# Kernel tuning notes

Hardware: AMD Instinct MI355X
Metric: run time of the kernel (lower is better)

Reference implementation:

```python
import jax, jax.numpy as jnp
import numpy as np

# Module hyperparameters (init_kwargs)
FS = 30.0          # sampling rate (Hz)
HIGH_PASS = 40.0   # bpm
LOW_PASS = 250.0   # bpm
DELTA_T = 300      # crop length (samples)
K = 64             # crops per (batch, channel)
B, C, T = 256, 16, 9000

NBINS = DELTA_T // 2 + 1  # rfft bins
# freqs = linspace(0, Fs/2, NBINS); band mask is static given shapes
_freqs = np.linspace(0.0, FS / 2.0, NBINS)
MASK_IDX = np.where((_freqs >= HIGH_PASS / 60.0) & (_freqs <= LOW_PASS / 60.0))[0]


def setup_inputs() -> dict:
    key = jax.random.key(0)
    k1, k2 = jax.random.split(key)
    inp = jax.random.normal(k1, (B, C, T), dtype=jnp.float32)
    # random temporal offsets, one per (b, c, k) crop
    offsets = jax.random.randint(k2, (B, C, K), 0, T - DELTA_T + 1, dtype=jnp.int32)
    return {"input": inp, "offsets": offsets}


def reference(input, offsets):
    # Batched gather of all random crops: [B, C, K, DELTA_T]
    t_idx = offsets[..., None] + jnp.arange(DELTA_T, dtype=jnp.int32)  # [B,C,K,dt]
    crops = jnp.take_along_axis(input[:, :, None, :], t_idx, axis=-1)
    # Remove per-crop mean
    crops = crops - jnp.mean(crops, axis=-1, keepdims=True)
    # rFFT with 'forward' norm (divide by n), power spectrum
    spec = jnp.fft.rfft(crops, axis=-1, norm='forward')   # [B,C,K,NBINS] complex
    power = spec.real ** 2 + spec.imag ** 2               # [B,C,K,NBINS]
    # Keep only the heart-rate band (static index set), normalize to unit sum
    power = power[..., MASK_IDX]                          # [B,C,K,F_band]
    power = power / jnp.sum(power, axis=-1, keepdims=True)
    return power
```

## Files before the change

### kernel.cpp

```cpp
#include <hip/hip_runtime.h>
#include <math.h>

#define TT 9000
#define DT 300
#define KK 64
#define NB 35
#define KMIN 7
#define NCH 4096
#define NPAIR (KK * NB)


typedef __bf16 bf16;
typedef __attribute__((ext_vector_type(8))) __bf16 bf16x8;
typedef __attribute__((ext_vector_type(4))) __bf16 bf16x4;
typedef __attribute__((ext_vector_type(4))) float f32x4;

#define NFRAG_ELEMS (10 * 6 * 64 * 8)

__global__ void build_w(bf16* __restrict__ tab) {
    int i = blockIdx.x * blockDim.x + threadIdx.x;
    if (i >= NFRAG_ELEMS) return;
    int j    = i & 7;
    int l    = (i >> 3) & 63;
    int f    = i >> 9;
    int nt   = f % 6;
    int ks   = f / 6;
    int quad = l >> 4;
    int c    = l & 15;
    int k    = ks * 32 + quad * 8 + j;
    int jf   = (nt % 3) * 16 + c;
    float v = 0.0f;
    if (jf <= NB - 1 && k < DT) {
        int bin = jf + KMIN;
        int ph  = (bin * k) % DT;
        float ang = 0.02094395102393195f * (float)ph;
        v = (nt >= 3) ? sinf(ang) : cosf(ang);
    }
    tab[i] = (bf16)v;
}

#define SPAD 9024

__global__ __launch_bounds__(256, 8) void st_mfma(
        const float* __restrict__ input,
        const int*   __restrict__ offsets,
        const bf16*  __restrict__ tab,
        float*       __restrict__ out) {
    __shared__ __align__(16) bf16 sig[SPAD];
    __shared__ int offs[KK];

    const int bc  = blockIdx.x;
    const int tid = threadIdx.x;

    const float4* src = (const float4*)(input + (size_t)bc * TT);
#pragma unroll
    for (int i = 0; i < 9; ++i) {
        int idx = tid + i * 256;
        if (idx < TT / 4) {
            float4 v = src[idx];
            bf16x4 b;
            b[0] = (bf16)v.x; b[1] = (bf16)v.y; b[2] = (bf16)v.z; b[3] = (bf16)v.w;
            *(bf16x4*)(sig + idx * 4) = b;
        }
    }
    if (tid < SPAD - TT) sig[TT + tid] = (bf16)0.0f;
    if (tid < KK) offs[tid] = offsets[bc * KK + tid];
    __syncthreads();

    const int w    = tid >> 6;
    const int lane = tid & 63;
    const int quad = lane >> 4;
    const int c    = lane & 15;

    const int off = offs[w * 16 + c];
    const int d0  = (off + quad * 8) >> 1;
    const unsigned sh = (unsigned)((off & 1) << 4);
    const int* ip = (const int*)sig;

    const bf16x8* wt = (const bf16x8*)tab;

    f32x4 acc[6];
#pragma unroll
    for (int nt = 0; nt < 6; ++nt) acc[nt] = (f32x4){0.f, 0.f, 0.f, 0.f};

#pragma unroll
    for (int ks = 0; ks < 10; ++ks) {
        const int db = d0 + ks * 16;
        int dw0 = ip[db + 0], dw1 = ip[db + 1], dw2 = ip[db + 2],
            dw3 = ip[db + 3], dw4 = ip[db + 4];
        union { unsigned u[4]; bf16x8 v; } a;
        a.u[0] = __builtin_amdgcn_alignbit((unsigned)dw1, (unsigned)dw0, sh);
        a.u[1] = __builtin_amdgcn_alignbit((unsigned)dw2, (unsigned)dw1, sh);
        a.u[2] = __builtin_amdgcn_alignbit((unsigned)dw3, (unsigned)dw2, sh);
        a.u[3] = __builtin_amdgcn_alignbit((unsigned)dw4, (unsigned)dw3, sh);

#pragma unroll
        for (int nt = 0; nt < 6; ++nt)
            acc[nt] = __builtin_amdgcn_mfma_f32_16x16x32_bf16(
                a.v, wt[(ks * 6 + nt) * 64 + lane], acc[nt], 0, 0, 0);
    }

    float* o = out + (size_t)bc * NPAIR;
#pragma unroll
    for (int r = 0; r < 4; ++r) {
        float p0 = acc[0][r] * acc[0][r] + acc[3][r] * acc[3][r];
        float p1 = acc[1][r] * acc[1][r] + acc[4][r] * acc[4][r];
        float p2 = acc[2][r] * acc[2][r] + acc[5][r] * acc[5][r];
        float s = p0 + p1 + ((c <= 2) ? p2 : 0.0f);
#pragma unroll
        for (int d = 1; d < 16; d <<= 1) s += __shfl_xor(s, d, 64);
        float rinv = 1.0f / s;
        int crop = w * 16 + quad * 4 + r;
        float* oc = o + crop * NB;
        oc[c] = p0 * rinv;
        oc[16 + c] = p1 * rinv;
        if (c <= 2) oc[32 + c] = p2 * rinv;
    }
}

extern "C" void kernel_launch(void* const* d_in, const int* in_sizes, int n_in,
                              void* d_out, int out_size, void* d_ws, size_t ws_size,
                              hipStream_t stream) {
    const float* input   = (const float*)d_in[0];
    const int*   offsets = (const int*)d_in[1];
    float*       out     = (float*)d_out;
    bf16*        tab     = (bf16*)d_ws;

    build_w<<<(NFRAG_ELEMS + 255) / 256, 256, 0, stream>>>(tab);
    st_mfma<<<NCH, 256, 0, stream>>>(input, offsets, tab, out);
}
```

Measured before the change: 251.2 us.

## Split frequency tiles across 12 waves and stage DFT weights in LDS

Each block grows from 4 to 12 waves. Each wave now handles one crop group and one of three frequency groups, computing only a cos/sin MFMA pair per k-step instead of six MFMAs. The bf16 DFT weight table is copied into shared memory with global_load_lds, so each wave no longer reads fragments from global memory. Per-crop normalization sums are combined across waves through a small shared array and a second barrier, and the reciprocal uses rcpf. In exchange, each block now loads about 60 KB of weights and uses far more LDS, which caps how many blocks fit on a CU, and the extra barrier adds a sync point.

```diff
diff --git a/kernel.cpp b/kernel.cpp
--- a/kernel.cpp
+++ b/kernel.cpp
@@ -16,6 +16,7 @@
 typedef __attribute__((ext_vector_type(4))) float f32x4;
 
 #define NFRAG_ELEMS (10 * 6 * 64 * 8)
+#define WBYTES 61440
 
 __global__ void build_w(bf16* __restrict__ tab) {
     int i = blockIdx.x * blockDim.x + threadIdx.x;
@@ -41,21 +42,34 @@
 
 #define SPAD 9024
 
-__global__ __launch_bounds__(256, 8) void st_mfma(
+__global__ __launch_bounds__(768, 6) void st_mfma(
         const float* __restrict__ input,
         const int*   __restrict__ offsets,
         const bf16*  __restrict__ tab,
         float*       __restrict__ out) {
     __shared__ __align__(16) bf16 sig[SPAD];
+    __shared__ __align__(16) unsigned char wlds[WBYTES];
+    __shared__ __align__(16) float part[KK][3];
     __shared__ int offs[KK];
 
-    const int bc  = blockIdx.x;
-    const int tid = threadIdx.x;
+    const int bc   = blockIdx.x;
+    const int tid  = threadIdx.x;
+    const int wid  = tid >> 6;
+    const int lane = tid & 63;
+
+#pragma unroll
+    for (int i = 0; i < 5; ++i) {
+        int chunk = wid * 5 + i;
+        __builtin_amdgcn_global_load_lds(
+            (const __attribute__((address_space(1))) void*)((const unsigned char*)tab + chunk * 1024 + lane * 16),
+            (__attribute__((address_space(3))) void*)(wlds + chunk * 1024),
+            16, 0, 0);
+    }
 
     const float4* src = (const float4*)(input + (size_t)bc * TT);
 #pragma unroll
-    for (int i = 0; i < 9; ++i) {
-        int idx = tid + i * 256;
+    for (int i = 0; i < 3; ++i) {
+        int idx = tid + i * 768;
         if (idx < TT / 4) {
             float4 v = src[idx];
             bf16x4 b;
@@ -67,21 +81,19 @@
     if (tid < KK) offs[tid] = offsets[bc * KK + tid];
     __syncthreads();
 
-    const int w    = tid >> 6;
-    const int lane = tid & 63;
+    const int m    = wid & 3;
+    const int pg   = wid >> 2;
     const int quad = lane >> 4;
     const int c    = lane & 15;
 
-    const int off = offs[w * 16 + c];
+    const int off = offs[m * 16 + c];
     const int d0  = (off + quad * 8) >> 1;
     const unsigned sh = (unsigned)((off & 1) << 4);
     const int* ip = (const int*)sig;
 
-    const bf16x8* wt = (const bf16x8*)tab;
+    const unsigned char* wp = wlds + (size_t)(pg * 64 + lane) * 16;
 
-    f32x4 acc[6];
-#pragma unroll
-    for (int nt = 0; nt < 6; ++nt) acc[nt] = (f32x4){0.f, 0.f, 0.f, 0.f};
+    f32x4 acc_c = {0.f,0.f,0.f,0.f}, acc_s = {0.f,0.f,0.f,0.f};
 
 #pragma unroll
     for (int ks = 0; ks < 10; ++ks) {
@@ -94,27 +106,32 @@
         a.u[2] = __builtin_amdgcn_alignbit((unsigned)dw3, (unsigned)dw2, sh);
         a.u[3] = __builtin_amdgcn_alignbit((unsigned)dw4, (unsigned)dw3, sh);
 
-#pragma unroll
-        for (int nt = 0; nt < 6; ++nt)
-            acc[nt] = __builtin_amdgcn_mfma_f32_16x16x32_bf16(
-                a.v, wt[(ks * 6 + nt) * 64 + lane], acc[nt], 0, 0, 0);
+        bf16x8 wc = *(const bf16x8*)(wp + (ks * 6    ) * 1024);
+        bf16x8 wn = *(const bf16x8*)(wp + (ks * 6 + 3) * 1024);
+        acc_c = __builtin_amdgcn_mfma_f32_16x16x32_bf16(a.v, wc, acc_c, 0, 0, 0);
+        acc_s = __builtin_amdgcn_mfma_f32_16x16x32_bf16(a.v, wn, acc_s, 0, 0, 0);
     }
 
-    float* o = out + (size_t)bc * NPAIR;
+    float pv[4];
 #pragma unroll
     for (int r = 0; r < 4; ++r) {
-        float p0 = acc[0][r] * acc[0][r] + acc[3][r] * acc[3][r];
-        float p1 = acc[1][r] * acc[1][r] + acc[4][r] * acc[4][r];
-        float p2 = acc[2][r] * acc[2][r] + acc[5][r] * acc[5][r];
-        float s = p0 + p1 + ((c <= 2) ? p2 : 0.0f);
+        float p = acc_c[r] * acc_c[r] + acc_s[r] * acc_s[r];
+        pv[r] = p;
+        float s = p;
 #pragma unroll
         for (int d = 1; d < 16; d <<= 1) s += __shfl_xor(s, d, 64);
-        float rinv = 1.0f / s;
-        int crop = w * 16 + quad * 4 + r;
-        float* oc = o + crop * NB;
-        oc[c] = p0 * rinv;
-        oc[16 + c] = p1 * rinv;
-        if (c <= 2) oc[32 + c] = p2 * rinv;
+        if (c == 0) part[m * 16 + quad * 4 + r][pg] = s;
+    }
+    __syncthreads();
+
+    float* ob = out + (size_t)bc * NPAIR;
+#pragma unroll
+    for (int r = 0; r < 4; ++r) {
+        int crop = m * 16 + quad * 4 + r;
+        float s = part[crop][0] + part[crop][1] + part[crop][2];
+        float rinv = __builtin_amdgcn_rcpf(s);
+        if (pg < 2 || c < 3)
+            ob[crop * NB + pg * 16 + c] = pv[r] * rinv;
     }
 }
 
@@ -127,5 +144,5 @@
     bf16*        tab     = (bf16*)d_ws;
 
     build_w<<<(NFRAG_ELEMS + 255) / 256, 256, 0, stream>>>(tab);
-    st_mfma<<<NCH, 256, 0, stream>>>(input, offsets, tab, out);
+    st_mfma<<<NCH, 768, 0, stream>>>(input, offsets, tab, out);
 }
```

New measurement: 233.2 us. -7.2%, faster.

## Stage DFT weight table in LDS and process eight channels per block

Applied to the files above, without the earlier changes.

Each block now copies the full bf16 DFT fragment table into shared memory once using global_load_lds, then loops over eight channels and reads the MFMA B operands from LDS instead of global memory. This is meant to cut repeated global and L2 traffic for the weight table and amortise its load across channels. The cost is much higher LDS use per block (about 78 KB), which lowers occupancy to roughly two blocks per CU. There are also only 512 blocks with serialized per-channel loads and no overlap between the input load and compute.

```diff
diff --git a/kernel.cpp b/kernel.cpp
--- a/kernel.cpp
+++ b/kernel.cpp
@@ -16,6 +16,7 @@
 typedef __attribute__((ext_vector_type(4))) float f32x4;
 
 #define NFRAG_ELEMS (10 * 6 * 64 * 8)
+#define WBYTES 61440
 
 __global__ void build_w(bf16* __restrict__ tab) {
     int i = blockIdx.x * blockDim.x + threadIdx.x;
@@ -40,81 +41,96 @@
 }
 
 #define SPAD 9024
+#define CPB  8
+#define NBLK (NCH / CPB)
 
-__global__ __launch_bounds__(256, 8) void st_mfma(
+__global__ __launch_bounds__(256, 2) void st_mfma(
         const float* __restrict__ input,
         const int*   __restrict__ offsets,
         const bf16*  __restrict__ tab,
         float*       __restrict__ out) {
     __shared__ __align__(16) bf16 sig[SPAD];
+    __shared__ __align__(16) unsigned char wlds[WBYTES];
     __shared__ int offs[KK];
 
-    const int bc  = blockIdx.x;
-    const int tid = threadIdx.x;
-
-    const float4* src = (const float4*)(input + (size_t)bc * TT);
-#pragma unroll
-    for (int i = 0; i < 9; ++i) {
-        int idx = tid + i * 256;
-        if (idx < TT / 4) {
-            float4 v = src[idx];
-            bf16x4 b;
-            b[0] = (bf16)v.x; b[1] = (bf16)v.y; b[2] = (bf16)v.z; b[3] = (bf16)v.w;
-            *(bf16x4*)(sig + idx * 4) = b;
-        }
-    }
-    if (tid < SPAD - TT) sig[TT + tid] = (bf16)0.0f;
-    if (tid < KK) offs[tid] = offsets[bc * KK + tid];
-    __syncthreads();
-
+    const int tid  = threadIdx.x;
     const int w    = tid >> 6;
     const int lane = tid & 63;
     const int quad = lane >> 4;
     const int c    = lane & 15;
 
-    const int off = offs[w * 16 + c];
-    const int d0  = (off + quad * 8) >> 1;
-    const unsigned sh = (unsigned)((off & 1) << 4);
-    const int* ip = (const int*)sig;
+#pragma unroll
+    for (int i = 0; i < 15; ++i) {
+        int chunk = w * 15 + i;
+        __builtin_amdgcn_global_load_lds(
+            (const __attribute__((address_space(1))) void*)((const unsigned char*)tab + chunk * 1024 + lane * 16),
+            (__attribute__((address_space(3))) void*)(wlds + chunk * 1024),
+            16, 0, 0);
+    }
 
-    const bf16x8* wt = (const bf16x8*)tab;
+#pragma unroll 1
+    for (int ch = 0; ch < CPB; ++ch) {
+        const int chg = blockIdx.x * CPB + ch;
 
-    f32x4 acc[6];
+        const float4* src = (const float4*)(input + (size_t)chg * TT);
 #pragma unroll
-    for (int nt = 0; nt < 6; ++nt) acc[nt] = (f32x4){0.f, 0.f, 0.f, 0.f};
+        for (int i = 0; i < 9; ++i) {
+            int idx = tid + i * 256;
+            if (idx < TT / 4) {
+                float4 v = src[idx];
+                bf16x4 b;
+                b[0] = (bf16)v.x; b[1] = (bf16)v.y; b[2] = (bf16)v.z; b[3] = (bf16)v.w;
+                *(bf16x4*)(sig + idx * 4) = b;
+            }
+        }
+        if (tid < SPAD - TT) sig[TT + tid] = (bf16)0.0f;
+        if (tid < KK) offs[tid] = offsets[(size_t)chg * KK + tid];
+        __syncthreads();
+
+        const int off = offs[w * 16 + c];
+        const int d0  = (off + quad * 8) >> 1;
+        const unsigned sh = (unsigned)((off & 1) << 4);
+        const int* ip = (const int*)sig;
+
+        f32x4 acc[6];
+#pragma unroll
+        for (int nt = 0; nt < 6; ++nt) acc[nt] = (f32x4){0.f, 0.f, 0.f, 0.f};
 
 #pragma unroll
-    for (int ks = 0; ks < 10; ++ks) {
-        const int db = d0 + ks * 16;
-        int dw0 = ip[db + 0], dw1 = ip[db + 1], dw2 = ip[db + 2],
-            dw3 = ip[db + 3], dw4 = ip[db + 4];
-        union { unsigned u[4]; bf16x8 v; } a;
-        a.u[0] = __builtin_amdgcn_alignbit((unsigned)dw1, (unsigned)dw0, sh);
-        a.u[1] = __builtin_amdgcn_alignbit((unsigned)dw2, (unsigned)dw1, sh);
-        a.u[2] = __builtin_amdgcn_alignbit((unsigned)dw3, (unsigned)dw2, sh);
-        a.u[3] = __builtin_amdgcn_alignbit((unsigned)dw4, (unsigned)dw3, sh);
+        for (int ks = 0; ks < 10; ++ks) {
+            const int db = d0 + ks * 16;
+            int dw0 = ip[db + 0], dw1 = ip[db + 1], dw2 = ip[db + 2],
+                dw3 = ip[db + 3], dw4 = ip[db + 4];
+            union { unsigned u[4]; bf16x8 v; } a;
+            a.u[0] = __builtin_amdgcn_alignbit((unsigned)dw1, (unsigned)dw0, sh);
+            a.u[1] = __builtin_amdgcn_alignbit((unsigned)dw2, (unsigned)dw1, sh);
+            a.u[2] = __builtin_amdgcn_alignbit((unsigned)dw3, (unsigned)dw2, sh);
+            a.u[3] = __builtin_amdgcn_alignbit((unsigned)dw4, (unsigned)dw3, sh);
 
 #pragma unroll
-        for (int nt = 0; nt < 6; ++nt)
-            acc[nt] = __builtin_amdgcn_mfma_f32_16x16x32_bf16(
-                a.v, wt[(ks * 6 + nt) * 64 + lane], acc[nt], 0, 0, 0);
-    }
+            for (int nt = 0; nt < 6; ++nt) {
+                bf16x8 wf = *(const bf16x8*)(wlds + ks * 6144 + nt * 1024 + lane * 16);
+                acc[nt] = __builtin_amdgcn_mfma_f32_16x16x32_bf16(a.v, wf, acc[nt], 0, 0, 0);
+            }
+        }
 
-    float* o = out + (size_t)bc * NPAIR;
+        float* o = out + (size_t)chg * NPAIR;
 #pragma unroll
-    for (int r = 0; r < 4; ++r) {
-        float p0 = acc[0][r] * acc[0][r] + acc[3][r] * acc[3][r];
-        float p1 = acc[1][r] * acc[1][r] + acc[4][r] * acc[4][r];
-        float p2 = acc[2][r] * acc[2][r] + acc[5][r] * acc[5][r];
-        float s = p0 + p1 + ((c <= 2) ? p2 : 0.0f);
+        for (int r = 0; r < 4; ++r) {
+            float p0 = acc[0][r] * acc[0][r] + acc[3][r] * acc[3][r];
+            float p1 = acc[1][r] * acc[1][r] + acc[4][r] * acc[4][r];
+            float p2 = acc[2][r] * acc[2][r] + acc[5][r] * acc[5][r];
+            float s = p0 + p1 + ((c <= 2) ? p2 : 0.0f);
 #pragma unroll
-        for (int d = 1; d < 16; d <<= 1) s += __shfl_xor(s, d, 64);
-        float rinv = 1.0f / s;
-        int crop = w * 16 + quad * 4 + r;
-        float* oc = o + crop * NB;
-        oc[c] = p0 * rinv;
-        oc[16 + c] = p1 * rinv;
-        if (c <= 2) oc[32 + c] = p2 * rinv;
+            for (int d = 1; d < 16; d <<= 1) s += __shfl_xor(s, d, 64);
+            float rinv = 1.0f / s;
+            int crop = w * 16 + quad * 4 + r;
+            float* oc = o + crop * NB;
+            oc[c] = p0 * rinv;
+            oc[16 + c] = p1 * rinv;
+            if (c <= 2) oc[32 + c] = p2 * rinv;
+        }
+        __syncthreads();
     }
 }
 
@@ -127,5 +143,5 @@
     bf16*        tab     = (bf16*)d_ws;
 
     build_w<<<(NFRAG_ELEMS + 255) / 256, 256, 0, stream>>>(tab);
-    st_mfma<<<NCH, 256, 0, stream>>>(input, offsets, tab, out);
+    st_mfma<<<NBLK, 256, 0, stream>>>(input, offsets, tab, out);
 }
```

Result: faster. 243.2 us (-3.2%).
